# Kernel tuning notes

Measured on AMD Instinct MI355X. Metric: run time of the kernel, lower is better.

Reference implementation:

```python
import jax, jax.numpy as jnp
import numpy as np

HEIGHT = 32
SIGMA = 2.0
NUM_NEGATIVE = 4096
N, C = 32, 512
L = HEIGHT * HEIGHT


def _grid_weight(height: int, sigma: float) -> jnp.ndarray:
    # distance_weights: pairwise Euclidean distance between grid points
    ii, jj = np.meshgrid(np.arange(height), np.arange(height), indexing='ij')
    coords = np.stack([ii.ravel(), jj.ravel()], axis=1).astype(np.float32)  # [L, 2]
    d2 = ((coords[:, None, :] - coords[None, :, :]) ** 2).sum(-1)  # squared dist [L, L]
    w = -(0.5 / sigma ** 2) * d2
    np.fill_diagonal(w, -np.inf)
    return jax.nn.softmax(jnp.asarray(w, dtype=jnp.float32), axis=1)


def setup_inputs() -> dict:
    key = jax.random.key(0)
    k1, k2 = jax.random.split(key)
    embedding = jax.random.normal(k1, (N, L, C), dtype=jnp.float32)
    weight = _grid_weight(HEIGHT, SIGMA)  # [L, L] softmax-normalized grid kernel
    neg_indices = jax.random.randint(k2, (NUM_NEGATIVE,), 0, N * L, dtype=jnp.int64)
    return {"embedding": embedding, "weight": weight, "neg_indices": neg_indices}


def reference(embedding, weight, neg_indices):
    n, l, c = embedding.shape
    # F.normalize(dim=-1), eps=1e-12
    norm = jnp.maximum(jnp.linalg.norm(embedding, axis=-1, keepdims=True), 1e-12)
    e = embedding / norm  # [N, L, C]
    # target = weight @ e  (broadcast over batch)
    target = jnp.einsum('kl,nlc->nkc', weight, e)  # [N, L, C]
    sim_pos = jnp.sum(e * target, axis=-1)  # [N, L]
    flat = e.reshape(-1, c)  # [N*L, C]
    negatives = flat[neg_indices]  # [M, C]
    sim_neg = jnp.einsum('nlc,mc->nlm', e, negatives)  # [N, L, M]
    logits = jnp.concatenate([sim_pos[..., None], sim_neg], axis=2).reshape(n * l, 1 + neg_indices.shape[0])
    # CrossEntropyLoss with target class 0, mean reduction
    loss = -jnp.mean(jax.nn.log_softmax(logits, axis=-1)[:, 0])
    return loss
```

## Files before the change

kernel.cpp:

```cpp
#include <hip/hip_runtime.h>
#include <hip/hip_bf16.h>
#include <stdint.h>

#define L_DIM 1024
#define C_DIM 512
#define CB4 256
#define N_BATCH 32
#define M_NEG 4096
#define NROWS (N_BATCH * L_DIM)

typedef float f32x4 __attribute__((ext_vector_type(4)));
typedef int i32x4 __attribute__((ext_vector_type(4)));
typedef int i32x8 __attribute__((ext_vector_type(8)));

#define E4_SCALE 32.0f
#define MX_SCALE 122
#define FMT_FP4 4

__device__ __forceinline__ void gl_lds16(const uint8_t* g, uint8_t* l) {
  __builtin_amdgcn_global_load_lds(
      (const __attribute__((address_space(1))) void*)g,
      (__attribute__((address_space(3))) void*)l, 16, 0, 0);
}

__device__ __forceinline__ uint32_t fp4_enc(float x) {
  const uint32_t s = (__float_as_uint(x) >> 31) << 3;
  const float a = fabsf(x);
  uint32_t c;
  c = a < 0.25f ? 0u
    : a < 0.75f ? 1u
    : a < 1.25f ? 2u
    : a < 1.75f ? 3u
    : a < 2.5f  ? 4u
    : a < 3.5f  ? 5u
    : a < 5.0f  ? 6u : 7u;
  return s | c;
}

__device__ __forceinline__ i32x8 fp4_op(i32x4 d) {
  return __builtin_shufflevector(d, d, 0, 1, 2, 3, -1, -1, -1, -1);
}

__global__ __launch_bounds__(256) void k_normalize(const float* __restrict__ emb,
                                                   uint8_t* __restrict__ out,
                                                   float* __restrict__ zerobuf,
                                                   float* __restrict__ loss_out) {
  if (blockIdx.x < 256) zerobuf[blockIdx.x * 256 + threadIdx.x] = 0.0f;
  if (blockIdx.x == 0 && threadIdx.x == 0) loss_out[0] = 0.0f;
  const int lane = threadIdx.x & 63;
  const int wave = threadIdx.x >> 6;
  const long row = (long)blockIdx.x * 4 + wave;
  const float4* src = (const float4*)(emb + row * C_DIM);
  float4 v0 = src[2 * lane];
  float4 v1 = src[2 * lane + 1];
  float ss = v0.x * v0.x + v0.y * v0.y + v0.z * v0.z + v0.w * v0.w +
             v1.x * v1.x + v1.y * v1.y + v1.z * v1.z + v1.w * v1.w;
#pragma unroll
  for (int off = 1; off < 64; off <<= 1) ss += __shfl_xor(ss, off, 64);
  const float s = E4_SCALE / fmaxf(sqrtf(ss), 1e-12f);
  uint32_t pk = fp4_enc(v0.x * s)        | (fp4_enc(v0.y * s) << 4) |
                (fp4_enc(v0.z * s) << 8) | (fp4_enc(v0.w * s) << 12) |
                (fp4_enc(v1.x * s) << 16)| (fp4_enc(v1.y * s) << 20) |
                (fp4_enc(v1.z * s) << 24)| (fp4_enc(v1.w * s) << 28);
  ((uint32_t*)(out + row * CB4))[lane] = pk;
}

__global__ __launch_bounds__(256, 2) void k_gemm_fused(
    const uint8_t* __restrict__ E4, const int* __restrict__ idx,
    const float* __restrict__ W, float* __restrict__ rowsum,
    float* __restrict__ simpos) {
  __shared__ __align__(16) unsigned char smem_raw[40960];
  uint8_t* sA = (uint8_t*)smem_raw;
  uint8_t* sB = sA + 256 * 64;

  const int tid = threadIdx.x;
  const int lane = tid & 63;
  const int wave = tid >> 6;
  const int wm = wave >> 1, wn = wave & 1;
  const int q = lane >> 4, c16 = lane & 15;

  const int bid = blockIdx.x;
  const bool is0 = bid >= 1024;
  long rowBase, colBase, n = 0;
  if (is0) {
    const int t = bid - 1024;
    const int xcd = t & 7, slot = t >> 3;
    rowBase = (long)(xcd * 16 + (slot & 15)) * 256;
    colBase = (long)(slot >> 4) * 128;
  } else {
    const int xcd = bid & 7, slot = bid >> 3;
    n = xcd * 4 + (slot & 3);
    const int inner = slot >> 2;
    rowBase = (long)(inner & 3) * 256;
    colBase = (long)(inner >> 2) * 128;
  }
  const long aBase = is0 ? rowBase : n * L_DIM + rowBase;

  long offA[4], offB[2];
#pragma unroll
  for (int r = 0; r < 4; ++r) {
    const int c = r * 256 + tid;
    const int rw = c >> 2, cb = c & 3;
    offA[r] = (aBase + rw) * CB4 + (cb ^ (rw & 3)) * 16;
  }
#pragma unroll
  for (int r = 0; r < 2; ++r) {
    const int c = r * 256 + tid;
    const int rw = c >> 2, cb = c & 3;
    const long bRow = is0 ? (long)idx[colBase + rw] : n * L_DIM + colBase + rw;
    offB[r] = bRow * CB4 + (cb ^ (rw & 3)) * 16;
  }

  f32x4 acc[8][4] = {};

#pragma unroll
  for (int ks = 0; ks < CB4; ks += 64) {
#pragma unroll
    for (int r = 0; r < 4; ++r)
      gl_lds16(E4 + offA[r] + ks, sA + (r * 256 + tid) * 16);
#pragma unroll
    for (int r = 0; r < 2; ++r)
      gl_lds16(E4 + offB[r] + ks, sB + (r * 256 + tid) * 16);
    __syncthreads();
    i32x8 bfr[4];
#pragma unroll
    for (int j = 0; j < 4; ++j) {
      const int row = wn * 64 + j * 16 + c16;
      bfr[j] = fp4_op(*(const i32x4*)(sB + row * 64 + (q ^ (row & 3)) * 16));
    }
#pragma unroll
    for (int i = 0; i < 8; ++i) {
      const int row = wm * 128 + i * 16 + c16;
      i32x8 af =
          fp4_op(*(const i32x4*)(sA + row * 64 + (q ^ (row & 3)) * 16));
#pragma unroll
      for (int j = 0; j < 4; ++j)
        acc[i][j] = __builtin_amdgcn_mfma_scale_f32_16x16x128_f8f6f4(
            af, bfr[j], acc[i][j], FMT_FP4, FMT_FP4,
            0, MX_SCALE, 0, MX_SCALE);
    }
    __syncthreads();
  }

  if (is0) {
    float* S = (float*)smem_raw;
#pragma unroll
    for (int i = 0; i < 8; ++i)
#pragma unroll
      for (int r = 0; r < 4; ++r) {
        const float s = __expf(acc[i][0][r]) + __expf(acc[i][1][r]) +
                        __expf(acc[i][2][r]) + __expf(acc[i][3][r]);
        S[wave * 2560 + (i * 16 + q * 4 + r) * 20 + c16] = s;
      }
    __syncthreads();
    {
      const int wmg = tid >> 7, rs = tid & 127;
      const float4* p0 = (const float4*)(S + (wmg * 2 + 0) * 2560 + rs * 20);
      const float4* p1 = (const float4*)(S + (wmg * 2 + 1) * 2560 + rs * 20);
      float4 t0 = p0[0], t1 = p0[1], t2 = p0[2], t3 = p0[3];
      float4 u0 = p1[0], u1 = p1[1], u2 = p1[2], u3 = p1[3];
      float v = t0.x + t0.y + t0.z + t0.w + t1.x + t1.y + t1.z + t1.w +
                t2.x + t2.y + t2.z + t2.w + t3.x + t3.y + t3.z + t3.w +
                u0.x + u0.y + u0.z + u0.w + u1.x + u1.y + u1.z + u1.w +
                u2.x + u2.y + u2.z + u2.w + u3.x + u3.y + u3.z + u3.w;
      atomicAdd(&rowsum[rowBase + tid], v);
    }
  } else {
    float* G = (float*)smem_raw;
#pragma unroll
    for (int p = 0; p < 4; ++p) {
      if (wm == (p >> 1)) {
        const int ib = (p & 1) * 4;
#pragma unroll
        for (int ii = 0; ii < 4; ++ii)
#pragma unroll
          for (int j = 0; j < 4; ++j)
#pragma unroll
            for (int r = 0; r < 4; ++r)
              G[(ii * 16 + q * 4 + r) * 132 + wn * 64 + j * 16 + c16] =
                  acc[ib + ii][j][r];
      }
      __syncthreads();
      {
        const int rr = tid >> 2;
        const int chunk = tid & 3;
        const long krow = rowBase + p * 64 + rr;
        float v = 0.0f;
#pragma unroll
        for (int u = 0; u < 8; ++u) {
          const float4 g = *(const float4*)(G + rr * 132 + u * 16 + chunk * 4);
          const float4 w4 =
              *(const float4*)(W + krow * L_DIM + colBase + u * 16 + chunk * 4);
          v += g.x * w4.x + g.y * w4.y + g.z * w4.z + g.w * w4.w;
        }
        v += __shfl_xor(v, 1, 64);
        v += __shfl_xor(v, 2, 64);
        if (chunk == 0) atomicAdd(&simpos[n * L_DIM + krow], v);
      }
      __syncthreads();
    }
  }
}

__global__ __launch_bounds__(256) void k_finalize(const float* __restrict__ rowsum,
                                                  const float* __restrict__ simpos,
                                                  float* __restrict__ out) {
  const int gid = blockIdx.x * 256 + threadIdx.x;
  const float sp = simpos[gid];
  float v = __logf(rowsum[gid] + __expf(sp)) - sp;
#pragma unroll
  for (int off = 1; off < 64; off <<= 1) v += __shfl_xor(v, off, 64);
  __shared__ float ws[4];
  if ((threadIdx.x & 63) == 0) ws[threadIdx.x >> 6] = v;
  __syncthreads();
  if (threadIdx.x == 0)
    atomicAdd(out, (ws[0] + ws[1] + ws[2] + ws[3]) * (1.0f / (float)NROWS));
}

extern "C" void kernel_launch(void* const* d_in, const int* in_sizes, int n_in,
                              void* d_out, int out_size, void* d_ws, size_t ws_size,
                              hipStream_t stream) {
  const float* emb = (const float*)d_in[0];
  const float* weight = (const float*)d_in[1];
  const int* negidx = (const int*)d_in[2];
  float* out = (float*)d_out;
  char* ws = (char*)d_ws;

  uint8_t* E4 = (uint8_t*)ws;
  float* rowsum = (float*)(ws + 8388608);
  float* simpos = (float*)(ws + 8519680);

  k_normalize<<<NROWS / 4, 256, 0, stream>>>(emb, E4, rowsum, out);
  k_gemm_fused<<<5120, 256, 0, stream>>>(E4, negidx, weight, rowsum, simpos);
  k_finalize<<<NROWS / 256, 256, 0, stream>>>(rowsum, simpos, out);
}
```

Measured before the change: 169.1 us.

## Shrink GEMM tile to 128x128 and load full K once into LDS

Changes the fused GEMM tile from 256x128 to 128x128 and doubles the grid. The whole K extent (256 bytes of FP4 per row) is loaded into LDS in one shot instead of a four-step K loop, which removes the per-step barriers. The LDS swizzle widens to 16 chunks, and the epilogues are adjusted for 64 rows per wave-row. In exchange, each tile reuses less data, so more A/B traffic and more atomics are generated, and the LDS footprint grows to 64KB, which may limit occupancy.

Result: slower. 189.0 us (+11.7%).

```diff
diff --git a/kernel.cpp b/kernel.cpp
--- a/kernel.cpp
+++ b/kernel.cpp
@@ -69,9 +69,9 @@
     const uint8_t* __restrict__ E4, const int* __restrict__ idx,
     const float* __restrict__ W, float* __restrict__ rowsum,
     float* __restrict__ simpos) {
-  __shared__ __align__(16) unsigned char smem_raw[40960];
+  __shared__ __align__(16) unsigned char smem_raw[65536];
   uint8_t* sA = (uint8_t*)smem_raw;
-  uint8_t* sB = sA + 256 * 64;
+  uint8_t* sB = sA + 128 * 256;
 
   const int tid = threadIdx.x;
   const int lane = tid & 63;
@@ -80,85 +80,91 @@
   const int q = lane >> 4, c16 = lane & 15;
 
   const int bid = blockIdx.x;
-  const bool is0 = bid >= 1024;
+  const bool is0 = bid >= 2048;
   long rowBase, colBase, n = 0;
   if (is0) {
-    const int t = bid - 1024;
+    const int t = bid - 2048;
     const int xcd = t & 7, slot = t >> 3;
-    rowBase = (long)(xcd * 16 + (slot & 15)) * 256;
-    colBase = (long)(slot >> 4) * 128;
+    rowBase = (long)(xcd * 32 + (slot & 31)) * 128;
+    colBase = (long)(slot >> 5) * 128;
   } else {
     const int xcd = bid & 7, slot = bid >> 3;
     n = xcd * 4 + (slot & 3);
     const int inner = slot >> 2;
-    rowBase = (long)(inner & 3) * 256;
-    colBase = (long)(inner >> 2) * 128;
+    rowBase = (long)(inner & 7) * 128;
+    colBase = (long)(inner >> 3) * 128;
   }
   const long aBase = is0 ? rowBase : n * L_DIM + rowBase;
 
-  long offA[4], offB[2];
-#pragma unroll
-  for (int r = 0; r < 4; ++r) {
+  long offB[8];
+#pragma unroll
+  for (int r = 0; r < 8; ++r) {
     const int c = r * 256 + tid;
-    const int rw = c >> 2, cb = c & 3;
-    offA[r] = (aBase + rw) * CB4 + (cb ^ (rw & 3)) * 16;
-  }
-#pragma unroll
-  for (int r = 0; r < 2; ++r) {
+    const int rw = c >> 4, cb = c & 15;
+    const long bRow = is0 ? (long)idx[colBase + rw] : n * L_DIM + colBase + rw;
+    offB[r] = bRow * CB4 + (cb ^ (rw & 15)) * 16;
+  }
+  long offA[8];
+#pragma unroll
+  for (int r = 0; r < 8; ++r) {
     const int c = r * 256 + tid;
-    const int rw = c >> 2, cb = c & 3;
-    const long bRow = is0 ? (long)idx[colBase + rw] : n * L_DIM + colBase + rw;
-    offB[r] = bRow * CB4 + (cb ^ (rw & 3)) * 16;
-  }
-
-  f32x4 acc[8][4] = {};
-
-#pragma unroll
-  for (int ks = 0; ks < CB4; ks += 64) {
-#pragma unroll
-    for (int r = 0; r < 4; ++r)
-      gl_lds16(E4 + offA[r] + ks, sA + (r * 256 + tid) * 16);
-#pragma unroll
-    for (int r = 0; r < 2; ++r)
-      gl_lds16(E4 + offB[r] + ks, sB + (r * 256 + tid) * 16);
-    __syncthreads();
+    const int rw = c >> 4, cb = c & 15;
+    offA[r] = (aBase + rw) * CB4 + (cb ^ (rw & 15)) * 16;
+  }
+
+#pragma unroll
+  for (int r = 0; r < 8; ++r)
+    gl_lds16(E4 + offB[r], sB + (r * 256 + tid) * 16);
+#pragma unroll
+  for (int r = 0; r < 8; ++r)
+    gl_lds16(E4 + offA[r], sA + (r * 256 + tid) * 16);
+  __syncthreads();
+
+  f32x4 acc[4][4] = {};
+
+#pragma unroll
+  for (int ks = 0; ks < 4; ++ks) {
+    const int ksl = ks * 4 + q;
     i32x8 bfr[4];
 #pragma unroll
     for (int j = 0; j < 4; ++j) {
       const int row = wn * 64 + j * 16 + c16;
-      bfr[j] = fp4_op(*(const i32x4*)(sB + row * 64 + (q ^ (row & 3)) * 16));
-    }
-#pragma unroll
-    for (int i = 0; i < 8; ++i) {
-      const int row = wm * 128 + i * 16 + c16;
+      bfr[j] =
+          fp4_op(*(const i32x4*)(sB + row * 256 + ((ksl ^ (row & 15)) * 16)));
+    }
+#pragma unroll
+    for (int i = 0; i < 4; ++i) {
+      const int row = wm * 64 + i * 16 + c16;
       i32x8 af =
-          fp4_op(*(const i32x4*)(sA + row * 64 + (q ^ (row & 3)) * 16));
+          fp4_op(*(const i32x4*)(sA + row * 256 + ((ksl ^ (row & 15)) * 16)));
 #pragma unroll
       for (int j = 0; j < 4; ++j)
         acc[i][j] = __builtin_amdgcn_mfma_scale_f32_16x16x128_f8f6f4(
             af, bfr[j], acc[i][j], FMT_FP4, FMT_FP4,
             0, MX_SCALE, 0, MX_SCALE);
     }
-    __syncthreads();
-  }
+  }
+  __syncthreads();
 
   if (is0) {
     float* S = (float*)smem_raw;
 #pragma unroll
-    for (int i = 0; i < 8; ++i)
+    for (int i = 0; i < 4; ++i)
 #pragma unroll
       for (int r = 0; r < 4; ++r) {
         const float s = __expf(acc[i][0][r]) + __expf(acc[i][1][r]) +
                         __expf(acc[i][2][r]) + __expf(acc[i][3][r]);
-        S[wave * 2560 + (i * 16 + q * 4 + r) * 20 + c16] = s;
+        S[wave * 1280 + (i * 16 + q * 4 + r) * 20 + c16] = s;
       }
     __syncthreads();
-    {
-      const int wmg = tid >> 7, rs = tid & 127;
-      const float4* p0 = (const float4*)(S + (wmg * 2 + 0) * 2560 + rs * 20);
-      const float4* p1 = (const float4*)(S + (wmg * 2 + 1) * 2560 + rs * 20);
-      float4 t0 = p0[0], t1 = p0[1], t2 = p0[2], t3 = p0[3];
-      float4 u0 = p1[0], u1 = p1[1], u2 = p1[2], u3 = p1[3];
+    if (tid < 128) {
+      const int wmr = tid >> 6, row64 = tid & 63;
+      const float* p0 = S + (wmr * 2 + 0) * 1280 + row64 * 20;
+      const float* p1 = S + (wmr * 2 + 1) * 1280 + row64 * 20;
+      float4 t0 = ((const float4*)p0)[0], t1 = ((const float4*)p0)[1];
+      float4 t2 = ((const float4*)p0)[2], t3 = ((const float4*)p0)[3];
+      float4 u0 = ((const float4*)p1)[0], u1 = ((const float4*)p1)[1];
+      float4 u2 = ((const float4*)p1)[2], u3 = ((const float4*)p1)[3];
       float v = t0.x + t0.y + t0.z + t0.w + t1.x + t1.y + t1.z + t1.w +
                 t2.x + t2.y + t2.z + t2.w + t3.x + t3.y + t3.z + t3.w +
                 u0.x + u0.y + u0.z + u0.w + u1.x + u1.y + u1.z + u1.w +
@@ -168,17 +174,16 @@
   } else {
     float* G = (float*)smem_raw;
 #pragma unroll
-    for (int p = 0; p < 4; ++p) {
-      if (wm == (p >> 1)) {
-        const int ib = (p & 1) * 4;
-#pragma unroll
-        for (int ii = 0; ii < 4; ++ii)
+    for (int p = 0; p < 2; ++p) {
+      if (wm == p) {
+#pragma unroll
+        for (int i = 0; i < 4; ++i)
 #pragma unroll
           for (int j = 0; j < 4; ++j)
 #pragma unroll
             for (int r = 0; r < 4; ++r)
-              G[(ii * 16 + q * 4 + r) * 132 + wn * 64 + j * 16 + c16] =
-                  acc[ib + ii][j][r];
+              G[(i * 16 + q * 4 + r) * 132 + wn * 64 + j * 16 + c16] =
+                  acc[i][j][r];
       }
       __syncthreads();
       {
@@ -231,6 +236,6 @@
   float* simpos = (float*)(ws + 8519680);
 
   k_normalize<<<NROWS / 4, 256, 0, stream>>>(emb, E4, rowsum, out);
-  k_gemm_fused<<<5120, 256, 0, stream>>>(E4, negidx, weight, rowsum, simpos);
+  k_gemm_fused<<<10240, 256, 0, stream>>>(E4, negidx, weight, rowsum, simpos);
   k_finalize<<<NROWS / 256, 256, 0, stream>>>(rowsum, simpos, out);
 }
```
